# Kernel tuning notes

Measured on AMD Instinct MI355X. Metric: run time of the kernel, lower is better.

Reference implementation:

```python
import jax, jax.numpy as jnp
import numpy as np

N, E = 100000, 1600000
IN_C, H, C = 256, 4, 64
NEG_SLOPE = 0.2


def setup_inputs() -> dict:
    key = jax.random.key(0)
    k1, k2, k3, k4, k5 = jax.random.split(key, 5)
    x = jax.random.normal(k1, (N, IN_C), dtype=jnp.float32)
    edge_index = jax.random.randint(k2, (2, E), 0, N, dtype=jnp.int64)
    # GATConv params: lin weight [IN_C, H*C], attention vectors [H, C], bias [C] (concat=False)
    W = jax.random.normal(k3, (IN_C, H * C), dtype=jnp.float32) / np.sqrt(IN_C)
    att_src = jax.random.normal(k4, (H, C), dtype=jnp.float32) / np.sqrt(C)
    att_dst = jax.random.normal(k5, (H, C), dtype=jnp.float32) / np.sqrt(C)
    bias = jnp.zeros((C,), dtype=jnp.float32)
    return {"x": x, "edge_index": edge_index, "W": W,
            "att_src": att_src, "att_dst": att_dst, "bias": bias}


def reference(x, edge_index, W, att_src, att_dst, bias):
    n = x.shape[0]
    # GATConv adds self-loops by default
    loops = jnp.arange(n, dtype=edge_index.dtype)
    src = jnp.concatenate([edge_index[0], loops])  # message source j
    dst = jnp.concatenate([edge_index[1], loops])  # message target i

    h = (x @ W).reshape(n, H, C)                       # [N,H,C]
    a_src = jnp.einsum('nhc,hc->nh', h, att_src)       # [N,H]
    a_dst = jnp.einsum('nhc,hc->nh', h, att_dst)       # [N,H]

    e = jax.nn.leaky_relu(a_src[src] + a_dst[dst], NEG_SLOPE)  # [E+N,H]
    m = jax.ops.segment_max(e, dst, num_segments=n)            # per-target max
    e = jnp.exp(e - m[dst])
    denom = jax.ops.segment_sum(e, dst, num_segments=n)
    alpha = e / (denom[dst] + 1e-16)                           # softmax over incoming edges

    out = jax.ops.segment_sum(alpha[:, :, None] * h[src], dst, num_segments=n)  # [N,H,C]
    return out.mean(axis=1) + bias  # concat=False -> mean over heads, [N,C]
```

## Files before the change

kernel.cpp:

```cpp
#include <hip/hip_runtime.h>

#define N_NODES 100000
#define N_EDGES 1600000
#define TOT (N_EDGES + N_NODES)
#define IN_CH 256
#define NHEAD 4
#define CH 64
#define HC 256
#define NEG_SLOPE 0.2f

typedef _Float16 half8 __attribute__((ext_vector_type(8)));
typedef _Float16 h2v __attribute__((ext_vector_type(2)));
typedef float f32x4 __attribute__((ext_vector_type(4)));
typedef unsigned short ushort_t;
typedef unsigned int uint_t;

static __device__ __forceinline__ ushort_t f2h(float f) {
  _Float16 h = (_Float16)f;
  return __builtin_bit_cast(ushort_t, h);
}

static __device__ __forceinline__ void gload_lds16(const char* g, char* l) {
  __builtin_amdgcn_global_load_lds(
      (const __attribute__((address_space(1))) unsigned int*)g,
      (__attribute__((address_space(3))) unsigned int*)l, 16, 0, 0);
}

__global__ __launch_bounds__(256) void conv_w(const float* __restrict__ W,
                                              uint4* __restrict__ Wt_arr) {
  int id = blockIdx.x * 256 + threadIdx.x;
  int lane = id & 63;
  int n = (id >> 6) & 15;
  int ks = id >> 10;
  int col = n * 16 + (lane & 15);
  int kbase = ks * 32 + (lane >> 4) * 8;
  ushort_t h[8];
#pragma unroll
  for (int j = 0; j < 8; ++j) h[j] = f2h(W[(size_t)(kbase + j) * HC + col]);
  uint4 u;
  u.x = (uint_t)h[0] | ((uint_t)h[1] << 16);
  u.y = (uint_t)h[2] | ((uint_t)h[3] << 16);
  u.z = (uint_t)h[4] | ((uint_t)h[5] << 16);
  u.w = (uint_t)h[6] | ((uint_t)h[7] << 16);
  Wt_arr[id] = u;
}

__global__ __launch_bounds__(512) void gemm_mfma(const float* __restrict__ X,
                                                 const uint4* __restrict__ Wt_arr,
                                                 const float* __restrict__ att_src,
                                                 const float* __restrict__ att_dst,
                                                 uint2* __restrict__ Hmp,
                                                 float* __restrict__ as_out,
                                                 float* __restrict__ ad_out, int M) {
  __shared__ uint4 Bs[2][1024];
  const int tid = threadIdx.x;
  const int lane = tid & 63;
  const int wid = tid >> 6;
  const int l16 = lane & 15;
  const int lhi = lane >> 4;
  const int row0 = blockIdx.x * 128;

  int rowA = row0 + wid * 16 + l16;
  if (rowA >= M) rowA = M - 1;
  const float* __restrict__ xr = X + (size_t)rowA * IN_CH + lhi * 8;

  const char* __restrict__ wsrc = (const char*)Wt_arr;
  char* bd0 = (char*)&Bs[0][0] + tid * 16;
  char* bd1 = (char*)&Bs[1][0] + tid * 16;

  gload_lds16(wsrc + tid * 16, bd0);
  gload_lds16(wsrc + 8192 + tid * 16, bd0 + 8192);
  float4 xa = *reinterpret_cast<const float4*>(xr);
  float4 xb = *reinterpret_cast<const float4*>(xr + 4);

  f32x4 acc[16] = {};
  int cur = 0;

#pragma unroll
  for (int ks = 0; ks < 8; ++ks) {
    __syncthreads();

    float4 na, nb;
    if (ks < 7) {
      char* bd = (cur == 0) ? bd1 : bd0;
      const char* s = wsrc + (ks + 1) * 16384 + tid * 16;
      gload_lds16(s, bd);
      gload_lds16(s + 8192, bd + 8192);
      na = *reinterpret_cast<const float4*>(xr + (ks + 1) * 32);
      nb = *reinterpret_cast<const float4*>(xr + (ks + 1) * 32 + 4);
    }

    uint4 ua;
    ua.x = __builtin_bit_cast(uint_t, __builtin_amdgcn_cvt_pkrtz(xa.x, xa.y));
    ua.y = __builtin_bit_cast(uint_t, __builtin_amdgcn_cvt_pkrtz(xa.z, xa.w));
    ua.z = __builtin_bit_cast(uint_t, __builtin_amdgcn_cvt_pkrtz(xb.x, xb.y));
    ua.w = __builtin_bit_cast(uint_t, __builtin_amdgcn_cvt_pkrtz(xb.z, xb.w));
    half8 a = __builtin_bit_cast(half8, ua);

    const char* bbase = (const char*)&Bs[cur][0];
#pragma unroll
    for (int n = 0; n < 16; ++n) {
      half8 b = *reinterpret_cast<const half8*>(bbase + n * 1024 + lane * 16);
      acc[n] = __builtin_amdgcn_mfma_f32_16x16x32_f16(a, b, acc[n], 0, 0, 0);
    }
    xa = na; xb = nb;
    cur ^= 1;
  }

  float attS[16], attD[16];
#pragma unroll
  for (int n = 0; n < 16; ++n) {
    attS[n] = att_src[n * 16 + l16];
    attD[n] = att_dst[n * 16 + l16];
  }

#pragma unroll
  for (int r = 0; r < 4; ++r) {
    int grow = row0 + wid * 16 + lhi * 4 + r;
    if (grow < M) {
#pragma unroll
      for (int n2 = 0; n2 < 4; ++n2) {
        uint_t pk01 = __builtin_bit_cast(uint_t,
            __builtin_amdgcn_cvt_pkrtz(acc[n2][r], acc[n2 + 4][r]));
        uint_t pk23 = __builtin_bit_cast(uint_t,
            __builtin_amdgcn_cvt_pkrtz(acc[n2 + 8][r], acc[n2 + 12][r]));
        Hmp[(size_t)grow * 64 + n2 * 16 + l16] = make_uint2(pk01, pk23);
      }
      float sv[4] = {0.f, 0.f, 0.f, 0.f}, dv[4] = {0.f, 0.f, 0.f, 0.f};
#pragma unroll
      for (int h = 0; h < 4; ++h)
#pragma unroll
        for (int j = 0; j < 4; ++j) {
          sv[h] += acc[h * 4 + j][r] * attS[h * 4 + j];
          dv[h] += acc[h * 4 + j][r] * attD[h * 4 + j];
        }
#pragma unroll
      for (int off = 1; off < 16; off <<= 1)
#pragma unroll
        for (int h = 0; h < 4; ++h) {
          sv[h] += __shfl_xor(sv[h], off, 16);
          dv[h] += __shfl_xor(dv[h], off, 16);
        }
      if (l16 == 0) {
#pragma unroll
        for (int h = 0; h < 4; ++h) {
          as_out[(size_t)grow * 4 + h] = sv[h];
          ad_out[(size_t)grow * 4 + h] = dv[h];
        }
      }
    }
  }
}

__global__ __launch_bounds__(256) void count_deg(const int* __restrict__ edst,
                                                 int* __restrict__ deg) {
  int t = blockIdx.x * 256 + threadIdx.x;
  if (t >= N_EDGES / 4) return;
  int4 d4 = reinterpret_cast<const int4*>(edst)[t];
  atomicAdd(&deg[d4.x], 1);
  atomicAdd(&deg[d4.y], 1);
  atomicAdd(&deg[d4.z], 1);
  atomicAdd(&deg[d4.w], 1);
}

__global__ __launch_bounds__(256) void scan1(const int* __restrict__ deg,
                                             int* __restrict__ rp,
                                             int* __restrict__ bsum) {
  __shared__ int sh[256];
  int t = threadIdx.x;
  int base = blockIdx.x * 1024 + t * 4;
  int v[4];
#pragma unroll
  for (int i = 0; i < 4; ++i) v[i] = (base + i < N_NODES) ? (deg[base + i] + 1) : 0;
  int tsum = v[0] + v[1] + v[2] + v[3];
  sh[t] = tsum;
  __syncthreads();
  for (int off = 1; off < 256; off <<= 1) {
    int x = (t >= off) ? sh[t - off] : 0;
    __syncthreads();
    sh[t] += x;
    __syncthreads();
  }
  if (t == 255) bsum[blockIdx.x] = sh[255];
  int run = sh[t] - tsum;
#pragma unroll
  for (int i = 0; i < 4; ++i) {
    if (base + i < N_NODES) rp[base + i] = run;
    run += v[i];
  }
}

#define NBLK1 ((N_NODES + 1023) / 1024)

__global__ __launch_bounds__(128) void scan2(const int* __restrict__ bsum,
                                             int* __restrict__ boff) {
  __shared__ int sh[128];
  int t = threadIdx.x;
  int own = (t < NBLK1) ? bsum[t] : 0;
  sh[t] = own;
  __syncthreads();
  for (int off = 1; off < 128; off <<= 1) {
    int x = (t >= off) ? sh[t - off] : 0;
    __syncthreads();
    sh[t] += x;
    __syncthreads();
  }
  boff[t] = sh[t] - own;
}

__global__ __launch_bounds__(256) void scan3(int* __restrict__ rp,
                                             const int* __restrict__ boff,
                                             int* __restrict__ cursor) {
  int idx = blockIdx.x * 256 + threadIdx.x;
  if (idx < N_NODES) {
    int v = rp[idx] + boff[idx >> 10];
    rp[idx] = v;
    cursor[idx] = v;
  }
  if (idx == 0) rp[N_NODES] = TOT;
}

__global__ __launch_bounds__(256) void scatter_edges(const int* __restrict__ esrc,
                                                     const int* __restrict__ edst,
                                                     const float* __restrict__ as_buf,
                                                     const float* __restrict__ ad_buf,
                                                     int* __restrict__ cursor,
                                                     uint4* __restrict__ erec) {
  int e = blockIdx.x * 256 + threadIdx.x;
  if (e >= TOT) return;
  if (e < 8) erec[TOT + e] = make_uint4(0u, 0u, 0u, 0u);
  int s, d;
  if (e < N_EDGES) { s = esrc[e]; d = edst[e]; }
  else { s = e - N_EDGES; d = s; }
  int p = atomicAdd(&cursor[d], 1);
  float4 a1 = *reinterpret_cast<const float4*>(as_buf + (size_t)s * NHEAD);
  float4 a2 = *reinterpret_cast<const float4*>(ad_buf + (size_t)d * NHEAD);
  float e0 = a1.x + a2.x; e0 = e0 > 0.f ? e0 : NEG_SLOPE * e0;
  float e1 = a1.y + a2.y; e1 = e1 > 0.f ? e1 : NEG_SLOPE * e1;
  float e2 = a1.z + a2.z; e2 = e2 > 0.f ? e2 : NEG_SLOPE * e2;
  float e3 = a1.w + a2.w; e3 = e3 > 0.f ? e3 : NEG_SLOPE * e3;
  float w0 = __expf(e0 - 4.f), w1 = __expf(e1 - 4.f);
  float w2 = __expf(e2 - 4.f), w3 = __expf(e3 - 4.f);
  uint_t pk01 = __builtin_bit_cast(uint_t, __builtin_amdgcn_cvt_pkrtz(w0, w1));
  uint_t pk23 = __builtin_bit_cast(uint_t, __builtin_amdgcn_cvt_pkrtz(w2, w3));
  erec[p] = make_uint4((uint_t)s, pk01, pk23, 0u);
}

__global__ __launch_bounds__(256) void aggregate(const int* __restrict__ rp,
                                                 const uint4* __restrict__ erec,
                                                 const uint2* __restrict__ Hp,
                                                 const float* __restrict__ bias,
                                                 float* __restrict__ out) {
  int n = blockIdx.x * 4 + (threadIdx.x >> 6);
  int lane = threadIdx.x & 63;
  if (n >= N_NODES) return;
  const int half = lane >> 5;
  const uint_t off_lane = (uint_t)(lane & 31) << 4;
  const char* __restrict__ Hb = (const char*)Hp;

  int beg = rp[n], end = rp[n + 1];

  float acc[8] = {};
  float den[4] = {};

  const uint4* __restrict__ ep = erec + beg + half;
  uint4 rec_a = ep[0];
  uint4 rec_b = ep[2];

  for (int j = beg; j < end; j += 4, ep += 4) {
    uint4 cur_a = rec_a;
    uint4 cur_b = rec_b;
    rec_a = ep[4];
    rec_b = ep[6];

    uint_t hoff_a = (cur_a.x << 9) | off_lane;
    uint_t hoff_b = (cur_b.x << 9) | off_lane;
    uint4 hva = *reinterpret_cast<const uint4*>(Hb + hoff_a);
    uint4 hvb = *reinterpret_cast<const uint4*>(Hb + hoff_b);

    bool act_a = (j + half) < end;
    bool act_b = (j + 2 + half) < end;
    uint_t wa01u = act_a ? cur_a.y : 0u;
    uint_t wa23u = act_a ? cur_a.z : 0u;
    uint_t wb01u = act_b ? cur_b.y : 0u;
    uint_t wb23u = act_b ? cur_b.z : 0u;

    h2v wa01 = __builtin_bit_cast(h2v, wa01u);
    h2v wa23 = __builtin_bit_cast(h2v, wa23u);
    h2v wb01 = __builtin_bit_cast(h2v, wb01u);
    h2v wb23 = __builtin_bit_cast(h2v, wb23u);

    h2v haa = __builtin_bit_cast(h2v, hva.x);
    h2v hab = __builtin_bit_cast(h2v, hva.y);
    h2v hac = __builtin_bit_cast(h2v, hva.z);
    h2v had = __builtin_bit_cast(h2v, hva.w);

    acc[0] += (float)wa01.x * (float)haa.x;
    acc[1] += (float)wa01.y * (float)haa.y;
    acc[2] += (float)wa23.x * (float)hab.x;
    acc[3] += (float)wa23.y * (float)hab.y;
    acc[4] += (float)wa01.x * (float)hac.x;
    acc[5] += (float)wa01.y * (float)hac.y;
    acc[6] += (float)wa23.x * (float)had.x;
    acc[7] += (float)wa23.y * (float)had.y;
    den[0] += (float)wa01.x;
    den[1] += (float)wa01.y;
    den[2] += (float)wa23.x;
    den[3] += (float)wa23.y;

    h2v hba = __builtin_bit_cast(h2v, hvb.x);
    h2v hbb = __builtin_bit_cast(h2v, hvb.y);
    h2v hbc = __builtin_bit_cast(h2v, hvb.z);
    h2v hbd = __builtin_bit_cast(h2v, hvb.w);

    acc[0] += (float)wb01.x * (float)hba.x;
    acc[1] += (float)wb01.y * (float)hba.y;
    acc[2] += (float)wb23.x * (float)hbb.x;
    acc[3] += (float)wb23.y * (float)hbb.y;
    acc[4] += (float)wb01.x * (float)hbc.x;
    acc[5] += (float)wb01.y * (float)hbc.y;
    acc[6] += (float)wb23.x * (float)hbd.x;
    acc[7] += (float)wb23.y * (float)hbd.y;
    den[0] += (float)wb01.x;
    den[1] += (float)wb01.y;
    den[2] += (float)wb23.x;
    den[3] += (float)wb23.y;
  }

#pragma unroll
  for (int k = 0; k < 8; ++k) acc[k] += __shfl_xor(acc[k], 32, 64);
#pragma unroll
  for (int k = 0; k < 4; ++k) den[k] += __shfl_xor(den[k], 32, 64);

  if (lane < 32) {
    float i0 = 1.f / (den[0] + 1e-30f);
    float i1 = 1.f / (den[1] + 1e-30f);
    float i2 = 1.f / (den[2] + 1e-30f);
    float i3 = 1.f / (den[3] + 1e-30f);
    float2 b2 = *reinterpret_cast<const float2*>(bias + 2 * lane);
    float rA = 0.25f * (acc[0] * i0 + acc[1] * i1 + acc[2] * i2 + acc[3] * i3) + b2.x;
    float rB = 0.25f * (acc[4] * i0 + acc[5] * i1 + acc[6] * i2 + acc[7] * i3) + b2.y;
    *reinterpret_cast<float2*>(out + (size_t)n * CH + 2 * lane) = make_float2(rA, rB);
  }
}

extern "C" void kernel_launch(void* const* d_in, const int* in_sizes, int n_in,
                              void* d_out, int out_size, void* d_ws, size_t ws_size,
                              hipStream_t stream) {
  const float* x       = (const float*)d_in[0];
  const int*   eidx    = (const int*)d_in[1];
  const float* W       = (const float*)d_in[2];
  const float* att_src = (const float*)d_in[3];
  const float* att_dst = (const float*)d_in[4];
  const float* bias    = (const float*)d_in[5];
  float* out = (float*)d_out;

  uint2* Hmp    = (uint2*)d_ws;
  uint4* erec   = (uint4*)(Hmp + (size_t)N_NODES * 64);
  float* as_buf = (float*)(erec + (size_t)TOT + 8);
  float* ad_buf = as_buf + (size_t)N_NODES * NHEAD;
  uint4* Wt_arr = (uint4*)(ad_buf + (size_t)N_NODES * NHEAD);
  int*   deg    = (int*)(Wt_arr + 8192);
  int*   rp     = deg + N_NODES;
  int*   bsum   = rp + N_NODES + 1;
  int*   boff   = bsum + 128;

  const int* esrc = eidx;
  const int* edst = eidx + N_EDGES;

  conv_w<<<32, 256, 0, stream>>>(W, Wt_arr);
  hipMemsetAsync(deg, 0, (size_t)N_NODES * sizeof(int), stream);
  count_deg<<<(N_EDGES / 4 + 255) / 256, 256, 0, stream>>>(edst, deg);

  dim3 ggrid((N_NODES + 127) / 128);
  gemm_mfma<<<ggrid, 512, 0, stream>>>(x, Wt_arr, att_src, att_dst, Hmp, as_buf, ad_buf,
                                       N_NODES);

  scan1<<<NBLK1, 256, 0, stream>>>(deg, rp, bsum);
  scan2<<<1, 128, 0, stream>>>(bsum, boff);
  scan3<<<(N_NODES + 255) / 256, 256, 0, stream>>>(rp, boff, deg );
  scatter_edges<<<(TOT + 255) / 256, 256, 0, stream>>>(esrc, edst, as_buf, ad_buf,
                                                       deg , erec);

  aggregate<<<(N_NODES + 3) / 4, 256, 0, stream>>>(rp, erec, Hmp, bias, out);
}
```

Before: 332.5 us.

## Stage X tiles through swizzled LDS via async loads and clamp aggregate prefetch

The GEMM now uses 256-thread blocks of 64 rows. X tiles are brought into double-buffered LDS with direct global-to-LDS loads and an XOR swizzle, replacing per-thread register prefetch of X, which is meant to improve load coalescing and overlap. The aggregate kernel clamps its prefetch indices to the node's last edge, so the zero padding records written by scatter_edges are no longer needed. This adds LDS use and more blocks, and the clamped prefetches issue redundant reads at segment ends.

Measured after the change: 328.7 us. About the same (-1.1%).

```diff
diff --git a/kernel.cpp b/kernel.cpp
--- a/kernel.cpp
+++ b/kernel.cpp
@@ -45,7 +45,7 @@
   Wt_arr[id] = u;
 }
 
-__global__ __launch_bounds__(512) void gemm_mfma(const float* __restrict__ X,
+__global__ __launch_bounds__(256) void gemm_mfma(const float* __restrict__ X,
                                                  const uint4* __restrict__ Wt_arr,
                                                  const float* __restrict__ att_src,
                                                  const float* __restrict__ att_dst,
@@ -53,25 +53,39 @@
                                                  float* __restrict__ as_out,
                                                  float* __restrict__ ad_out, int M) {
   __shared__ uint4 Bs[2][1024];
+  __shared__ __align__(16) float As[2][2048];
   const int tid = threadIdx.x;
   const int lane = tid & 63;
   const int wid = tid >> 6;
   const int l16 = lane & 15;
   const int lhi = lane >> 4;
-  const int row0 = blockIdx.x * 128;
-
-  int rowA = row0 + wid * 16 + l16;
-  if (rowA >= M) rowA = M - 1;
-  const float* __restrict__ xr = X + (size_t)rowA * IN_CH + lhi * 8;
+  const int row0 = blockIdx.x * 64;
+
+  const int arow = tid >> 3;
+  const int aslot = tid & 7;
+  int ga0 = row0 + arow;       if (ga0 >= M) ga0 = M - 1;
+  int ga1 = row0 + arow + 32;  if (ga1 >= M) ga1 = M - 1;
+  const int sslot = aslot ^ (arow & 7);
+  const char* asrc0 = (const char*)X + (size_t)ga0 * 1024 + (sslot << 4);
+  const char* asrc1 = (const char*)X + (size_t)ga1 * 1024 + (sslot << 4);
+  char* adst0 = (char*)&As[0][0] + tid * 16;
+  char* adst1 = (char*)&As[1][0] + tid * 16;
 
   const char* __restrict__ wsrc = (const char*)Wt_arr;
   char* bd0 = (char*)&Bs[0][0] + tid * 16;
   char* bd1 = (char*)&Bs[1][0] + tid * 16;
 
-  gload_lds16(wsrc + tid * 16, bd0);
-  gload_lds16(wsrc + 8192 + tid * 16, bd0 + 8192);
-  float4 xa = *reinterpret_cast<const float4*>(xr);
-  float4 xb = *reinterpret_cast<const float4*>(xr + 4);
+  const int frow = wid * 16 + l16;
+  const int sw = frow & 7;
+  const int fo0 = frow * 32 + (((2 * lhi + 0) ^ sw) << 2);
+  const int fo1 = frow * 32 + (((2 * lhi + 1) ^ sw) << 2);
+
+  gload_lds16(asrc0, adst0);
+  gload_lds16(asrc1, adst0 + 4096);
+  gload_lds16(wsrc + tid * 16,         bd0);
+  gload_lds16(wsrc + 4096 + tid * 16,  bd0 + 4096);
+  gload_lds16(wsrc + 8192 + tid * 16,  bd0 + 8192);
+  gload_lds16(wsrc + 12288 + tid * 16, bd0 + 12288);
 
   f32x4 acc[16] = {};
   int cur = 0;
@@ -80,21 +94,26 @@
   for (int ks = 0; ks < 8; ++ks) {
     __syncthreads();
 
-    float4 na, nb;
     if (ks < 7) {
+      char* ad = (cur == 0) ? adst1 : adst0;
+      gload_lds16(asrc0 + (ks + 1) * 128, ad);
+      gload_lds16(asrc1 + (ks + 1) * 128, ad + 4096);
       char* bd = (cur == 0) ? bd1 : bd0;
       const char* s = wsrc + (ks + 1) * 16384 + tid * 16;
-      gload_lds16(s, bd);
-      gload_lds16(s + 8192, bd + 8192);
-      na = *reinterpret_cast<const float4*>(xr + (ks + 1) * 32);
-      nb = *reinterpret_cast<const float4*>(xr + (ks + 1) * 32 + 4);
+      gload_lds16(s,         bd);
+      gload_lds16(s + 4096,  bd + 4096);
+      gload_lds16(s + 8192,  bd + 8192);
+      gload_lds16(s + 12288, bd + 12288);
     }
 
+    const float* Ab = &As[cur][0];
+    float4 f0 = *reinterpret_cast<const float4*>(Ab + fo0);
+    float4 f1 = *reinterpret_cast<const float4*>(Ab + fo1);
     uint4 ua;
-    ua.x = __builtin_bit_cast(uint_t, __builtin_amdgcn_cvt_pkrtz(xa.x, xa.y));
-    ua.y = __builtin_bit_cast(uint_t, __builtin_amdgcn_cvt_pkrtz(xa.z, xa.w));
-    ua.z = __builtin_bit_cast(uint_t, __builtin_amdgcn_cvt_pkrtz(xb.x, xb.y));
-    ua.w = __builtin_bit_cast(uint_t, __builtin_amdgcn_cvt_pkrtz(xb.z, xb.w));
+    ua.x = __builtin_bit_cast(uint_t, __builtin_amdgcn_cvt_pkrtz(f0.x, f0.y));
+    ua.y = __builtin_bit_cast(uint_t, __builtin_amdgcn_cvt_pkrtz(f0.z, f0.w));
+    ua.z = __builtin_bit_cast(uint_t, __builtin_amdgcn_cvt_pkrtz(f1.x, f1.y));
+    ua.w = __builtin_bit_cast(uint_t, __builtin_amdgcn_cvt_pkrtz(f1.z, f1.w));
     half8 a = __builtin_bit_cast(half8, ua);
 
     const char* bbase = (const char*)&Bs[cur][0];
@@ -103,7 +122,6 @@
       half8 b = *reinterpret_cast<const half8*>(bbase + n * 1024 + lane * 16);
       acc[n] = __builtin_amdgcn_mfma_f32_16x16x32_f16(a, b, acc[n], 0, 0, 0);
     }
-    xa = na; xb = nb;
     cur ^= 1;
   }
 
@@ -228,7 +246,6 @@
                                                      uint4* __restrict__ erec) {
   int e = blockIdx.x * 256 + threadIdx.x;
   if (e >= TOT) return;
-  if (e < 8) erec[TOT + e] = make_uint4(0u, 0u, 0u, 0u);
   int s, d;
   if (e < N_EDGES) { s = esrc[e]; d = edst[e]; }
   else { s = e - N_EDGES; d = s; }
@@ -259,19 +276,23 @@
   const char* __restrict__ Hb = (const char*)Hp;
 
   int beg = rp[n], end = rp[n + 1];
+  const int last = end - 1;
 
   float acc[8] = {};
   float den[4] = {};
 
-  const uint4* __restrict__ ep = erec + beg + half;
-  uint4 rec_a = ep[0];
-  uint4 rec_b = ep[2];
-
-  for (int j = beg; j < end; j += 4, ep += 4) {
+  int ia = beg + half;     if (ia > last) ia = last;
+  int ib = beg + 2 + half; if (ib > last) ib = last;
+  uint4 rec_a = erec[ia];
+  uint4 rec_b = erec[ib];
+
+  for (int j = beg; j < end; j += 4) {
     uint4 cur_a = rec_a;
     uint4 cur_b = rec_b;
-    rec_a = ep[4];
-    rec_b = ep[6];
+    ia = j + 4 + half; if (ia > last) ia = last;
+    ib = j + 6 + half; if (ib > last) ib = last;
+    rec_a = erec[ia];
+    rec_b = erec[ib];
 
     uint_t hoff_a = (cur_a.x << 9) | off_lane;
     uint_t hoff_b = (cur_b.x << 9) | off_lane;
@@ -372,8 +393,8 @@
   hipMemsetAsync(deg, 0, (size_t)N_NODES * sizeof(int), stream);
   count_deg<<<(N_EDGES / 4 + 255) / 256, 256, 0, stream>>>(edst, deg);
 
-  dim3 ggrid((N_NODES + 127) / 128);
-  gemm_mfma<<<ggrid, 512, 0, stream>>>(x, Wt_arr, att_src, att_dst, Hmp, as_buf, ad_buf,
+  dim3 ggrid((N_NODES + 63) / 64);
+  gemm_mfma<<<ggrid, 256, 0, stream>>>(x, Wt_arr, att_src, att_dst, Hmp, as_buf, ad_buf,
                                        N_NODES);
 
   scan1<<<NBLK1, 256, 0, stream>>>(deg, rp, bsum);
```
